# Optimization experiments

Measured on AMD Instinct MI355X. Metric: run time of the kernel, lower is better.

## Reference

```python
import jax, jax.numpy as jnp
import numpy as np

POS_R, NEG_MIN_R, NEG_MAX_R, NEG_STEP = 3, 7, 8, 2
CELL_D, BORDER, MAX_NEG_B = 8, 16, 8


def _offsets():
    pos = np.array([(i, j) for i in range(-POS_R, POS_R + 1)
                    for j in range(-POS_R, POS_R + 1)
                    if i * i + j * j <= POS_R ** 2], dtype=np.int32).T  # [2, 29]
    neg = np.array([(i, j) for i in range(-NEG_MAX_R, NEG_MAX_R + 1, NEG_STEP)
                    for j in range(-NEG_MAX_R, NEG_MAX_R + 1, NEG_STEP)
                    if NEG_MIN_R ** 2 <= i * i + j * j <= NEG_MAX_R ** 2], dtype=np.int32).T  # [2, 12]
    return jnp.asarray(pos), jnp.asarray(neg)


def _sample(det, max_b=None):
    # pixel_unshuffle(det[:, :, t:-t, t:-t], cell_d) + argmax over the cell_d^2 channel dim,
    # then decode argmax index back to absolute (x=col, y=row) coordinates.
    B = det.shape[0] if max_b is None else min(max_b, det.shape[0])
    H, W = det.shape[2], det.shape[3]
    d, t = CELL_D, BORDER
    inner = det[:B, 0, t:H - t, t:W - t]                      # [B, Hc, Wc]
    hc, wc = (H - 2 * t) // d, (W - 2 * t) // d
    # pixel_unshuffle channel order is (row_offset i) major, (col_offset j) minor
    cells = inner.reshape(B, hc, d, wc, d).transpose(0, 1, 3, 2, 4).reshape(B, hc, wc, d * d)
    idx = jnp.argmax(cells, axis=-1)                          # [B, hc, wc]
    ii, jj = idx // d, idx % d                                # row / col offsets inside cell
    cy = jnp.arange(hc, dtype=jnp.int32)[None, :, None]
    cx = jnp.arange(wc, dtype=jnp.int32)[None, None, :]
    x = (t + cx * d + jj).reshape(-1)                         # column coordinate (unit_aflow channel 0)
    y = (t + cy * d + ii).reshape(-1)                         # row coordinate   (unit_aflow channel 1)
    n = hc * wc
    b = jnp.repeat(jnp.arange(B, dtype=jnp.int32), n)
    return b, x, y, n


def reference(output1, output2, aflow):
    des1, det1, qlt1 = output1[:, :128], output1[:, 128:129] if False else None, None  # placeholder
    raise NotImplementedError


# NOTE: forward args are the unpacked tensors (see setup_inputs keys)

def _forward(des1, det1, qlt1, des2, det2, qlt2, aflow):
    B, _, H, W = aflow.shape
    pos_off, neg_off = _offsets()
    # original code unpacks sample()'s (b, x, y, n) as (b, y1, x1, n) -- kept faithfully
    b, y1, x1, n = _sample(det1)
    s_des1 = des1[b, :, y1, x1]                               # [N, D]
    xy2 = (aflow[b, :, y1, x1] + 0.5).astype(jnp.int32).T     # [2, N]
    mask = ((0 <= xy2[0]) & (0 <= xy2[1]) & (xy2[0] < W) & (xy2[1] < H)).reshape(B, n)

    def clamp(xy):
        return jnp.stack([jnp.clip(xy[0], 0, W - 1), jnp.clip(xy[1], 0, H - 1)])

    xy2p = clamp(xy2[:, None, :] + pos_off[:, :, None])       # [2, P, N]
    gpos = des2[b, :, xy2p[1], xy2p[0]]                       # [P, N, D]
    pall = jnp.einsum('nd,pnd->np', s_des1, gpos)             # [N, P]
    pos = jnp.argmax(pall, axis=1)                            # [N]
    pscores = jnp.max(pall, axis=1, keepdims=True)            # [N, 1]
    sel_xy2 = clamp(xy2 + pos_off[:, pos])                    # [2, N]
    qlt = (qlt1[b, :, y1, x1] + qlt2[b, :, sel_xy2[1], sel_xy2[0]]) / 2  # [N, 1]

    xy2n = clamp(xy2[:, None, :] + neg_off[:, :, None])       # [2, Q, N]
    nscores = jnp.einsum('nd,qnd->nq', s_des1, des2[b, :, xy2n[1], xy2n[0]])  # [N, Q]

    bd, yd, xd, _ = _sample(det2, MAX_NEG_B)                  # same unpack swap as original
    distr = des2[bd, :, yd, xd]                               # [Nd, D]
    dscores = s_des1 @ distr.T                                # [N, Nd]
    dis2 = (xd[None, :] - xy2[0][:, None]) ** 2 + (yd[None, :] - xy2[1][:, None]) ** 2
    dis2 = dis2 + (bd[None, :] != b[:, None]).astype(jnp.int32) * POS_R ** 2
    dscores = jnp.where(dis2 < POS_R ** 2, 0.0, dscores)

    scores = jnp.concatenate([pscores, nscores, dscores], axis=1)
    labels = jnp.zeros(scores.shape, dtype=bool).at[:, :1].set(True)
    return scores, labels, mask, qlt


def setup_inputs() -> dict:
    key = jax.random.key(0)
    ks = jax.random.split(key, 7)
    B, D, H, W = 8, 128, 256, 256
    des1 = jax.random.normal(ks[0], (B, D, H, W), jnp.float32)
    det1 = jax.random.normal(ks[1], (B, 1, H, W), jnp.float32)
    qlt1 = jax.random.uniform(ks[2], (B, 1, H, W), jnp.float32)
    des2 = jax.random.normal(ks[3], (B, D, H, W), jnp.float32)
    det2 = jax.random.normal(ks[4], (B, 1, H, W), jnp.float32)
    qlt2 = jax.random.uniform(ks[5], (B, 1, H, W), jnp.float32)
    # absolute flow in pixel units, slightly out of range so the validity mask is exercised
    aflow = jax.random.uniform(ks[6], (B, 2, H, W), jnp.float32) * (W + 40.0) - 20.0
    return {"des1": des1, "det1": det1, "qlt1": qlt1,
            "des2": des2, "det2": det2, "qlt2": qlt2, "aflow": aflow}


def reference(des1, det1, qlt1, des2, det2, qlt2, aflow):
    return _forward(des1, det1, qlt1, des2, det2, qlt2, aflow)
```

## Files before the change

### kernel.cpp

```cpp
#include <hip/hip_runtime.h>

typedef unsigned short u16;
typedef unsigned int u32;
typedef __bf16 bf16x8 __attribute__((ext_vector_type(8)));
typedef float f32x4 __attribute__((ext_vector_type(4)));
typedef unsigned int u32x4 __attribute__((ext_vector_type(4)));

#define NS 6272
#define NCOLS 6285
#define SCORES_OFF 0LL
#define LABELS_OFF 39419520LL
#define MASK_OFF   78839040LL
#define QLT_OFF    78845312LL

#define ZBLK 2048
#define LBL_F4 9854880

__constant__ int POSX[29] = {-3,-2,-2,-2,-2,-2,-1,-1,-1,-1,-1, 0,0,0,0,0,0,0, 1,1,1,1,1, 2,2,2,2,2, 3};
__constant__ int POSY[29] = { 0,-2,-1, 0, 1, 2,-2,-1, 0, 1, 2,-3,-2,-1,0,1,2,3,-2,-1,0,1,2,-2,-1,0,1,2, 0};
__constant__ int NEGX[12] = {-8,-6,-6,-4,-4, 0,0, 4,4, 6,6, 8};
__constant__ int NEGY[12] = { 0,-4, 4,-6, 6,-8,8,-6,6,-4,4, 0};

__device__ inline u16 f2bf(float f) {
  u32 u = __float_as_uint(f);
  u = (u + 0x7FFFu + ((u >> 16) & 1u)) >> 16;
  return (u16)u;
}

__global__ __launch_bounds__(256) void sample_gather_zero_kernel(
    const float* __restrict__ det1, const float* __restrict__ det2,
    const float* __restrict__ aflow, const float* __restrict__ qlt1,
    const float* __restrict__ des1, const float* __restrict__ des2,
    int* __restrict__ x2a, int* __restrict__ y2a,
    int* __restrict__ xd, int* __restrict__ yd,
    float* __restrict__ qlt1v,
    float* __restrict__ A_f32, u16* __restrict__ A_bf16, u16* __restrict__ D_bf16,
    float* __restrict__ out) {
  if (blockIdx.x >= 3136) {
    size_t t = (size_t)(blockIdx.x - 3136) * 256 + threadIdx.x;
    f32x4* p = (f32x4*)(out + LABELS_OFF);
    f32x4 z = {0.0f, 0.0f, 0.0f, 0.0f};
    for (size_t i = t; i < (size_t)LBL_F4; i += (size_t)ZBLK * 256)
      __builtin_nontemporal_store(z, p + i);
    return;
  }
  int isDet2 = (blockIdx.x >= 1568);
  int cell = (blockIdx.x - (isDet2 ? 1568 : 0)) * 4 + (threadIdx.x >> 6);
  int l = threadIdx.x & 63;
  int b = cell / 784, rem = cell % 784;
  int cy = rem / 28, cx = rem % 28;
  int y = 16 + cy * 8 + (l >> 3), x = 16 + cx * 8 + (l & 7);
  const float* det = isDet2 ? det2 : det1;
  float v = det[((size_t)b << 16) + (y << 8) + x];
  int idx = l;
  #pragma unroll
  for (int off = 1; off < 64; off <<= 1) {
    float ov = __shfl_xor(v, off);
    int oi = __shfl_xor(idx, off);
    if (ov > v || (ov == v && oi < idx)) { v = ov; idx = oi; }
  }
  int ii = idx >> 3, jj = idx & 7;
  int X = 16 + cx * 8 + jj;
  int Y = 16 + cy * 8 + ii;
  if (!isDet2) {
    if (l == 0) {
      float ax = aflow[((size_t)(b * 2) << 16) + (X << 8) + Y];
      float ay = aflow[((size_t)(b * 2 + 1) << 16) + (X << 8) + Y];
      int xx = (int)(ax + 0.5f);
      int yy = (int)(ay + 0.5f);
      x2a[cell] = xx; y2a[cell] = yy;
      out[MASK_OFF + cell] = (xx >= 0 && yy >= 0 && xx < 256 && yy < 256) ? 1.0f : 0.0f;
      qlt1v[cell] = qlt1[((size_t)b << 16) + (X << 8) + Y];
    }
    const float* p = des1 + (((size_t)b * 128) << 16) + (X << 8) + Y;
    float v0 = p[(size_t)l << 16];
    float v1 = p[(size_t)(l + 64) << 16];
    A_f32[(size_t)cell * 128 + l] = v0;
    A_f32[(size_t)cell * 128 + l + 64] = v1;
    A_bf16[(size_t)cell * 128 + l] = f2bf(v0);
    A_bf16[(size_t)cell * 128 + l + 64] = f2bf(v1);
  } else {
    if (l == 0) {
      yd[cell] = X; xd[cell] = Y;
    }
    const float* p = des2 + (((size_t)b * 128) << 16) + (X << 8) + Y;
    D_bf16[(size_t)cell * 128 + l] = f2bf(p[(size_t)l << 16]);
    D_bf16[(size_t)cell * 128 + l + 64] = f2bf(p[(size_t)(l + 64) << 16]);
  }
}

__global__ __launch_bounds__(256, 2) void scores_kernel(
    const u16* __restrict__ A, const u16* __restrict__ Bm,
    const float* __restrict__ des2, const float* __restrict__ qlt2,
    const float* __restrict__ A_f32, const float* __restrict__ qlt1v,
    const int* __restrict__ x2a, const int* __restrict__ y2a,
    const int* __restrict__ xd, const int* __restrict__ yd,
    float* __restrict__ out) {
  __shared__ u16 As[128 * 136];
  __shared__ u16 Bs[128 * 136];
  int tid = threadIdx.x;
  if (blockIdx.x < 1568) {
    int n = blockIdx.x * 4 + (tid >> 6);
    int l = tid & 63;
    int b = n / 784;
    int x2 = x2a[n], y2 = y2a[n];
    int ox = 0, oy = 0;
    if (l < 29) { ox = POSX[l]; oy = POSY[l]; }
    else if (l < 41) { ox = NEGX[l - 29]; oy = NEGY[l - 29]; }
    int xc = min(max(x2 + ox, 0), 255);
    int yc = min(max(y2 + oy, 0), 255);
    const float* d2 = des2 + ((size_t)b << 23) + ((size_t)yc << 8) + xc;
    const float* ar = A_f32 + (size_t)n * 128;
    float acc = 0.0f;
    #pragma unroll 16
    for (int c = 0; c < 128; ++c) acc += ar[c] * d2[(size_t)c << 16];
    if (l >= 29 && l < 41) out[SCORES_OFF + (size_t)n * NCOLS + 1 + (l - 29)] = acc;
    float v = (l < 29) ? acc : -1e30f;
    int idx = l;
    #pragma unroll
    for (int off = 32; off; off >>= 1) {
      float ov = __shfl_down(v, off);
      int oi = __shfl_down(idx, off);
      if (ov > v || (ov == v && oi < idx)) { v = ov; idx = oi; }
    }
    if (l == 0) {
      out[SCORES_OFF + (size_t)n * NCOLS] = v;
      out[LABELS_OFF + (size_t)n * NCOLS] = 1.0f;
      int sx = min(max(x2 + POSX[idx], 0), 255);
      int sy = min(max(y2 + POSY[idx], 0), 255);
      float q = (qlt1v[n] + qlt2[((size_t)b << 16) + (sy << 8) + sx]) * 0.5f;
      out[QLT_OFF + n] = q;
    }
    return;
  }
  int bi = blockIdx.x - 1568;
  int R = bi / 49, C = bi % 49;
  const u32x4* gA = (const u32x4*)(A + (size_t)R * 16384);
  const u32x4* gB = (const u32x4*)(Bm + (size_t)C * 16384);
  #pragma unroll
  for (int p = 0; p < 8; ++p) {
    int i = tid + p * 256;
    int r = i >> 4, kc = (i & 15) * 8;
    *(u32x4*)&As[r * 136 + kc] = gA[i];
    *(u32x4*)&Bs[r * 136 + kc] = gB[i];
  }
  __syncthreads();
  int l = tid & 63, w = tid >> 6;
  int lr = l & 15, lq = l >> 4;
  int wr = (w & 1) * 64, wc = (w >> 1) * 64;
  f32x4 acc[4][4] = {};
  #pragma unroll
  for (int kk = 0; kk < 4; ++kk) {
    bf16x8 af[4], bfr[4];
    #pragma unroll
    for (int t = 0; t < 4; ++t) {
      af[t]  = *(const bf16x8*)&As[(wr + t * 16 + lr) * 136 + kk * 32 + lq * 8];
      bfr[t] = *(const bf16x8*)&Bs[(wc + t * 16 + lr) * 136 + kk * 32 + lq * 8];
    }
    #pragma unroll
    for (int tr = 0; tr < 4; ++tr)
      #pragma unroll
      for (int tc = 0; tc < 4; ++tc)
        acc[tr][tc] = __builtin_amdgcn_mfma_f32_16x16x32_bf16(af[tr], bfr[tc], acc[tr][tc], 0, 0, 0);
  }
  #pragma unroll
  for (int tr = 0; tr < 4; ++tr) {
    int rows[4], rx[4], ry[4], rb[4];
    #pragma unroll
    for (int r = 0; r < 4; ++r) {
      int row = R * 128 + wr + tr * 16 + lq * 4 + r;
      rows[r] = row; rx[r] = x2a[row]; ry[r] = y2a[row]; rb[r] = row / 784;
    }
    #pragma unroll
    for (int tc = 0; tc < 4; ++tc) {
      int col = C * 128 + wc + tc * 16 + lr;
      int cxv = xd[col], cyv = yd[col], cb = col / 784;
      #pragma unroll
      for (int r = 0; r < 4; ++r) {
        int dx = cxv - rx[r], dy = cyv - ry[r];
        int dis2 = dx * dx + dy * dy + (cb != rb[r] ? 9 : 0);
        float v = acc[tr][tc][r];
        if (dis2 < 9) v = 0.0f;
        __builtin_nontemporal_store(v, &out[SCORES_OFF + (size_t)rows[r] * NCOLS + 13 + col]);
      }
    }
  }
}

extern "C" void kernel_launch(void* const* d_in, const int* in_sizes, int n_in,
                              void* d_out, int out_size, void* d_ws, size_t ws_size,
                              hipStream_t stream) {
  const float* des1 = (const float*)d_in[0];
  const float* det1 = (const float*)d_in[1];
  const float* qlt1 = (const float*)d_in[2];
  const float* des2 = (const float*)d_in[3];
  const float* det2 = (const float*)d_in[4];
  const float* qlt2 = (const float*)d_in[5];
  const float* aflow = (const float*)d_in[6];
  float* out = (float*)d_out;

  char* ws = (char*)d_ws;
  int* x2a = (int*)ws;
  int* y2a = x2a + NS;
  int* xd  = y2a + NS;
  int* yd  = xd + NS;
  float* qlt1v = (float*)(yd + NS);
  float* A_f32 = qlt1v + NS + NS;
  u16* A_bf16 = (u16*)(A_f32 + (size_t)NS * 128);
  u16* D_bf16 = A_bf16 + (size_t)NS * 128;

  sample_gather_zero_kernel<<<3136 + ZBLK, 256, 0, stream>>>(
      det1, det2, aflow, qlt1, des1, des2,
      x2a, y2a, xd, yd, qlt1v, A_f32, A_bf16, D_bf16, out);

  scores_kernel<<<1568 + 49 * 49, 256, 0, stream>>>(
      A_bf16, D_bf16, des2, qlt2, A_f32, qlt1v, x2a, y2a, xd, yd, out);
}
```

Measured before the change: 811.9 us.

## Transpose des2 to channel-last workspace, swizzle LDS, stage score tiles for coalesced stores

When the workspace is large enough, the first kernel also writes a full channel-last copy of des2 (256 MB) through shared memory. The positive/negative score gather can then read contiguous 128-float vectors per pixel with 8 lanes per offset, instead of one strided load per channel. The GEMM path switches its LDS layout from padding to an XOR swizzle. It also stages each output tile through shared memory so score rows are written coalesced. The trade is a large extra read and write of des2 to produce the transpose, which only pays off if the strided gather was the main cost.

```diff
diff --git a/kernel.cpp b/kernel.cpp
--- a/kernel.cpp
+++ b/kernel.cpp
@@ -15,11 +15,13 @@
 
 #define ZBLK 2048
 #define LBL_F4 9854880
-
-__constant__ int POSX[29] = {-3,-2,-2,-2,-2,-2,-1,-1,-1,-1,-1, 0,0,0,0,0,0,0, 1,1,1,1,1, 2,2,2,2,2, 3};
-__constant__ int POSY[29] = { 0,-2,-1, 0, 1, 2,-2,-1, 0, 1, 2,-3,-2,-1,0,1,2,3,-2,-1,0,1,2,-2,-1,0,1,2, 0};
-__constant__ int NEGX[12] = {-8,-6,-6,-4,-4, 0,0, 4,4, 6,6, 8};
-__constant__ int NEGY[12] = { 0,-4, 4,-6, 6,-8,8,-6,6,-4,4, 0};
+#define TBLK 16384
+#define DES2T_BYTES 268435456ull
+
+__constant__ int OFFX[41] = {-3,-2,-2,-2,-2,-2,-1,-1,-1,-1,-1, 0,0,0,0,0,0,0, 1,1,1,1,1, 2,2,2,2,2, 3,
+                             -8,-6,-6,-4,-4, 0,0, 4,4, 6,6, 8};
+__constant__ int OFFY[41] = { 0,-2,-1, 0, 1, 2,-2,-1, 0, 1, 2,-3,-2,-1,0,1,2,3,-2,-1,0,1,2,-2,-1,0,1,2, 0,
+                              0,-4, 4,-6, 6,-8,8,-6,6,-4,4, 0};
 
 __device__ inline u16 f2bf(float f) {
   u32 u = __float_as_uint(f);
@@ -27,7 +29,8 @@
   return (u16)u;
 }
 
-__global__ __launch_bounds__(256) void sample_gather_zero_kernel(
+template <int USE_T>
+__global__ __launch_bounds__(256) void k1_kernel(
     const float* __restrict__ det1, const float* __restrict__ det2,
     const float* __restrict__ aflow, const float* __restrict__ qlt1,
     const float* __restrict__ des1, const float* __restrict__ des2,
@@ -35,7 +38,29 @@
     int* __restrict__ xd, int* __restrict__ yd,
     float* __restrict__ qlt1v,
     float* __restrict__ A_f32, u16* __restrict__ A_bf16, u16* __restrict__ D_bf16,
-    float* __restrict__ out) {
+    float* __restrict__ des2T, float* __restrict__ out) {
+  __shared__ float sm[32 * 129];
+  if (USE_T && blockIdx.x >= 5184) {
+    int tb = blockIdx.x - 5184;
+    int b = tb >> 11, y = (tb >> 3) & 255, x0 = (tb & 7) * 32;
+    int t = threadIdx.x;
+    int xi = t & 31, cb = t >> 5;
+    #pragma unroll
+    for (int p = 0; p < 16; ++p) {
+      int c = cb + p * 8;
+      sm[xi * 129 + c] = des2[(((size_t)(b * 128 + c)) << 16) + (y << 8) + x0 + xi];
+    }
+    __syncthreads();
+    int c2 = t & 127, xb = t >> 7;
+    size_t obase = ((((size_t)b << 16) + (y << 8) + x0) << 7);
+    #pragma unroll
+    for (int q = 0; q < 16; ++q) {
+      int xw = xb + 2 * q;
+      __builtin_nontemporal_store(sm[xw * 129 + c2],
+                                  &des2T[obase + ((size_t)xw << 7) + c2]);
+    }
+    return;
+  }
   if (blockIdx.x >= 3136) {
     size_t t = (size_t)(blockIdx.x - 3136) * 256 + threadIdx.x;
     f32x4* p = (f32x4*)(out + LABELS_OFF);
@@ -89,73 +114,116 @@
   }
 }
 
-__global__ __launch_bounds__(256, 2) void scores_kernel(
+template <int USE_T>
+__global__ __launch_bounds__(256, 2) void k2_kernel(
     const u16* __restrict__ A, const u16* __restrict__ Bm,
     const float* __restrict__ des2, const float* __restrict__ qlt2,
     const float* __restrict__ A_f32, const float* __restrict__ qlt1v,
     const int* __restrict__ x2a, const int* __restrict__ y2a,
     const int* __restrict__ xd, const int* __restrict__ yd,
-    float* __restrict__ out) {
-  __shared__ u16 As[128 * 136];
-  __shared__ u16 Bs[128 * 136];
+    const float* __restrict__ des2T, float* __restrict__ out) {
+  __shared__ __align__(16) char smem[66560];
   int tid = threadIdx.x;
   if (blockIdx.x < 1568) {
     int n = blockIdx.x * 4 + (tid >> 6);
     int l = tid & 63;
     int b = n / 784;
     int x2 = x2a[n], y2 = y2a[n];
-    int ox = 0, oy = 0;
-    if (l < 29) { ox = POSX[l]; oy = POSY[l]; }
-    else if (l < 41) { ox = NEGX[l - 29]; oy = NEGY[l - 29]; }
-    int xc = min(max(x2 + ox, 0), 255);
-    int yc = min(max(y2 + oy, 0), 255);
-    const float* d2 = des2 + ((size_t)b << 23) + ((size_t)yc << 8) + xc;
-    const float* ar = A_f32 + (size_t)n * 128;
-    float acc = 0.0f;
-    #pragma unroll 16
-    for (int c = 0; c < 128; ++c) acc += ar[c] * d2[(size_t)c << 16];
-    if (l >= 29 && l < 41) out[SCORES_OFF + (size_t)n * NCOLS + 1 + (l - 29)] = acc;
-    float v = (l < 29) ? acc : -1e30f;
-    int idx = l;
-    #pragma unroll
-    for (int off = 32; off; off >>= 1) {
-      float ov = __shfl_down(v, off);
-      int oi = __shfl_down(idx, off);
-      if (ov > v || (ov == v && oi < idx)) { v = ov; idx = oi; }
-    }
-    if (l == 0) {
-      out[SCORES_OFF + (size_t)n * NCOLS] = v;
-      out[LABELS_OFF + (size_t)n * NCOLS] = 1.0f;
-      int sx = min(max(x2 + POSX[idx], 0), 255);
-      int sy = min(max(y2 + POSY[idx], 0), 255);
-      float q = (qlt1v[n] + qlt2[((size_t)b << 16) + (sy << 8) + sx]) * 0.5f;
-      out[QLT_OFF + n] = q;
+    if (USE_T) {
+      const f32x4* av = (const f32x4*)(A_f32 + (size_t)n * 128);
+      int o = l & 7;
+      f32x4 a0 = av[o], a1 = av[o + 8], a2 = av[o + 16], a3 = av[o + 24];
+      float best = -1e30f; int bestk = 63;
+      #pragma unroll
+      for (int pass = 0; pass < 6; ++pass) {
+        int k = pass * 8 + (l >> 3);
+        int kc = min(k, 40);
+        int xc = min(max(x2 + OFFX[kc], 0), 255);
+        int yc = min(max(y2 + OFFY[kc], 0), 255);
+        const f32x4* d = (const f32x4*)(des2T + ((((size_t)b << 16) + (yc << 8) + xc) << 7));
+        f32x4 d0 = d[o], d1 = d[o + 8], d2v = d[o + 16], d3 = d[o + 24];
+        float s = a0[0]*d0[0] + a0[1]*d0[1] + a0[2]*d0[2] + a0[3]*d0[3]
+                + a1[0]*d1[0] + a1[1]*d1[1] + a1[2]*d1[2] + a1[3]*d1[3]
+                + a2[0]*d2v[0] + a2[1]*d2v[1] + a2[2]*d2v[2] + a2[3]*d2v[3]
+                + a3[0]*d3[0] + a3[1]*d3[1] + a3[2]*d3[2] + a3[3]*d3[3];
+        s += __shfl_xor(s, 1); s += __shfl_xor(s, 2); s += __shfl_xor(s, 4);
+        if (k <= 28) {
+          if (s > best) { best = s; bestk = k; }
+        } else if (k <= 40 && o == 0) {
+          out[SCORES_OFF + (size_t)n * NCOLS + 1 + (k - 29)] = s;
+        }
+      }
+      #pragma unroll
+      for (int off = 8; off < 64; off <<= 1) {
+        float ov = __shfl_xor(best, off);
+        int ok = __shfl_xor(bestk, off);
+        if (ov > best || (ov == best && ok < bestk)) { best = ov; bestk = ok; }
+      }
+      if (l == 0) {
+        out[SCORES_OFF + (size_t)n * NCOLS] = best;
+        out[LABELS_OFF + (size_t)n * NCOLS] = 1.0f;
+        int sx = min(max(x2 + OFFX[bestk], 0), 255);
+        int sy = min(max(y2 + OFFY[bestk], 0), 255);
+        out[QLT_OFF + n] = (qlt1v[n] + qlt2[((size_t)b << 16) + (sy << 8) + sx]) * 0.5f;
+      }
+    } else {
+      int ox = 0, oy = 0;
+      if (l < 41) { ox = OFFX[l]; oy = OFFY[l]; }
+      int xc = min(max(x2 + ox, 0), 255);
+      int yc = min(max(y2 + oy, 0), 255);
+      const float* d2 = des2 + ((size_t)b << 23) + ((size_t)yc << 8) + xc;
+      const float* ar = A_f32 + (size_t)n * 128;
+      float acc = 0.0f;
+      #pragma unroll 16
+      for (int c = 0; c < 128; ++c) acc += ar[c] * d2[(size_t)c << 16];
+      if (l >= 29 && l < 41) out[SCORES_OFF + (size_t)n * NCOLS + 1 + (l - 29)] = acc;
+      float v = (l < 29) ? acc : -1e30f;
+      int idx = l;
+      #pragma unroll
+      for (int off = 32; off; off >>= 1) {
+        float ov = __shfl_down(v, off);
+        int oi = __shfl_down(idx, off);
+        if (ov > v || (ov == v && oi < idx)) { v = ov; idx = oi; }
+      }
+      if (l == 0) {
+        out[SCORES_OFF + (size_t)n * NCOLS] = v;
+        out[LABELS_OFF + (size_t)n * NCOLS] = 1.0f;
+        int sx = min(max(x2 + OFFX[idx], 0), 255);
+        int sy = min(max(y2 + OFFY[idx], 0), 255);
+        out[QLT_OFF + n] = (qlt1v[n] + qlt2[((size_t)b << 16) + (sy << 8) + sx]) * 0.5f;
+      }
     }
     return;
   }
+  u16* As = (u16*)smem;
+  u16* Bs = As + 16384;
   int bi = blockIdx.x - 1568;
   int R = bi / 49, C = bi % 49;
   const u32x4* gA = (const u32x4*)(A + (size_t)R * 16384);
   const u32x4* gB = (const u32x4*)(Bm + (size_t)C * 16384);
+  u32x4* wA = (u32x4*)As; u32x4* wB = (u32x4*)Bs;
   #pragma unroll
   for (int p = 0; p < 8; ++p) {
     int i = tid + p * 256;
-    int r = i >> 4, kc = (i & 15) * 8;
-    *(u32x4*)&As[r * 136 + kc] = gA[i];
-    *(u32x4*)&Bs[r * 136 + kc] = gB[i];
+    int r = i >> 4, cc = i & 15;
+    int sw = r * 16 + (cc ^ (r & 7));
+    wA[sw] = gA[i];
+    wB[sw] = gB[i];
   }
   __syncthreads();
   int l = tid & 63, w = tid >> 6;
   int lr = l & 15, lq = l >> 4;
   int wr = (w & 1) * 64, wc = (w >> 1) * 64;
+  int sw7 = lr & 7;
   f32x4 acc[4][4] = {};
   #pragma unroll
   for (int kk = 0; kk < 4; ++kk) {
     bf16x8 af[4], bfr[4];
+    int cc = ((kk * 4 + lq) ^ sw7) * 8;
     #pragma unroll
     for (int t = 0; t < 4; ++t) {
-      af[t]  = *(const bf16x8*)&As[(wr + t * 16 + lr) * 136 + kk * 32 + lq * 8];
-      bfr[t] = *(const bf16x8*)&Bs[(wc + t * 16 + lr) * 136 + kk * 32 + lq * 8];
+      af[t]  = *(const bf16x8*)&As[(wr + t * 16 + lr) * 128 + cc];
+      bfr[t] = *(const bf16x8*)&Bs[(wc + t * 16 + lr) * 128 + cc];
     }
     #pragma unroll
     for (int tr = 0; tr < 4; ++tr)
@@ -163,6 +231,8 @@
       for (int tc = 0; tc < 4; ++tc)
         acc[tr][tc] = __builtin_amdgcn_mfma_f32_16x16x32_bf16(af[tr], bfr[tc], acc[tr][tc], 0, 0, 0);
   }
+  __syncthreads();
+  float* Cs = (float*)smem;
   #pragma unroll
   for (int tr = 0; tr < 4; ++tr) {
     int rows[4], rx[4], ry[4], rb[4];
@@ -181,9 +251,18 @@
         int dis2 = dx * dx + dy * dy + (cb != rb[r] ? 9 : 0);
         float v = acc[tr][tc][r];
         if (dis2 < 9) v = 0.0f;
-        __builtin_nontemporal_store(v, &out[SCORES_OFF + (size_t)rows[r] * NCOLS + 13 + col]);
-      }
-    }
+        Cs[(wr + tr * 16 + lq * 4 + r) * 130 + wc + tc * 16 + lr] = v;
+      }
+    }
+  }
+  __syncthreads();
+  size_t base = (size_t)R * 128 * NCOLS + 13 + (size_t)C * 128;
+  int rr = tid >> 7, c = tid & 127;
+  #pragma unroll 8
+  for (int p = 0; p < 64; ++p) {
+    int row = rr + 2 * p;
+    __builtin_nontemporal_store(Cs[row * 130 + c],
+                                &out[SCORES_OFF + base + (size_t)row * NCOLS + c]);
   }
 }
 
@@ -199,20 +278,32 @@
   const float* aflow = (const float*)d_in[6];
   float* out = (float*)d_out;
 
+  const size_t need = DES2T_BYTES + 6598144ull;
+  const bool useT = (ws_size >= need);
+
   char* ws = (char*)d_ws;
-  int* x2a = (int*)ws;
+  float* des2T = (float*)ws;
+  char* wsb = ws + (useT ? DES2T_BYTES : 0);
+  int* x2a = (int*)wsb;
   int* y2a = x2a + NS;
   int* xd  = y2a + NS;
   int* yd  = xd + NS;
   float* qlt1v = (float*)(yd + NS);
-  float* A_f32 = qlt1v + NS + NS;
+  float* A_f32 = qlt1v + 2 * NS;
   u16* A_bf16 = (u16*)(A_f32 + (size_t)NS * 128);
   u16* D_bf16 = A_bf16 + (size_t)NS * 128;
 
-  sample_gather_zero_kernel<<<3136 + ZBLK, 256, 0, stream>>>(
-      det1, det2, aflow, qlt1, des1, des2,
-      x2a, y2a, xd, yd, qlt1v, A_f32, A_bf16, D_bf16, out);
-
-  scores_kernel<<<1568 + 49 * 49, 256, 0, stream>>>(
-      A_bf16, D_bf16, des2, qlt2, A_f32, qlt1v, x2a, y2a, xd, yd, out);
+  if (useT) {
+    k1_kernel<1><<<3136 + ZBLK + TBLK, 256, 0, stream>>>(
+        det1, det2, aflow, qlt1, des1, des2,
+        x2a, y2a, xd, yd, qlt1v, A_f32, A_bf16, D_bf16, des2T, out);
+    k2_kernel<1><<<1568 + 49 * 49, 256, 0, stream>>>(
+        A_bf16, D_bf16, des2, qlt2, A_f32, qlt1v, x2a, y2a, xd, yd, des2T, out);
+  } else {
+    k1_kernel<0><<<3136 + ZBLK, 256, 0, stream>>>(
+        det1, det2, aflow, qlt1, des1, des2,
+        x2a, y2a, xd, yd, qlt1v, A_f32, A_bf16, D_bf16, des2T, out);
+    k2_kernel<0><<<1568 + 49 * 49, 256, 0, stream>>>(
+        A_bf16, D_bf16, des2, qlt2, A_f32, qlt1v, x2a, y2a, xd, yd, des2T, out);
+  }
 }
```

Result: faster. 729.6 us (-10.1%).
